# Kernel tuning notes

Hardware: AMD Instinct MI355X
Metric: run time of the kernel (lower is better)

## Reference

```python
import jax, jax.numpy as jnp
import numpy as np

BIG_NUM = 1000000000.0

def setup_inputs() -> dict:
    key0 = jax.random.key(0)
    k1, k2, k3, k4 = jax.random.split(key0, 4)
    B, T, D = 64, 4096, 512
    query = jax.random.normal(k1, (B, D), dtype=jnp.float32)
    key = jax.random.normal(k2, (B, T, D), dtype=jnp.float32)
    value = jax.random.normal(k3, (B, T, D), dtype=jnp.float32)
    mask = jax.random.randint(k4, (B, T), 0, 2, dtype=jnp.int32)
    return {"query": query, "key": key, "value": value, "mask": mask}

def reference(query, key, value, mask):
    # query: [B, D], key/value: [B, T, D], mask: [B, T] (1 = keep, 0 = mask)
    D = query.shape[1]
    scale = D ** 0.5
    # energy[b, t] = key[b, t, :] . query[b, :]
    energy = jnp.einsum('btd,bd->bt', key, query) / scale
    energy = energy + (mask.astype(jnp.float32) - 1.0) * BIG_NUM
    attn = jax.nn.softmax(energy, axis=-1)          # [B, T]
    context = jnp.einsum('bt,btd->bd', attn, value)  # [B, D]
    return (context, attn)
```

## Files before the change

kernel.cpp:

```cpp
#include <hip/hip_runtime.h>
#include <math.h>

#define B 64
#define T 4096
#define D 512
#define NCH 32
#define CHT (T / NCH)
#define WSTRIP 32
#define KBATCH 4
#define VBATCH 8

typedef __attribute__((address_space(1))) const void global_cv;
typedef __attribute__((address_space(3))) void lds_v;

__device__ __forceinline__ float wave_sum64(float v) {
#pragma unroll
    for (int off = 32; off; off >>= 1)
        v += __shfl_xor(v, off, 64);
    return v;
}

__device__ __forceinline__ void stage_row(const float* __restrict__ gsrc_row,
                                          float* lds_row, int lane) {
    __builtin_amdgcn_global_load_lds((global_cv*)(gsrc_row + lane * 4),
                                     (lds_v*)(lds_row), 16, 0, 0);
    __builtin_amdgcn_global_load_lds((global_cv*)(gsrc_row + 256 + lane * 4),
                                     (lds_v*)(lds_row + 256), 16, 0, 0);
}

__global__ __launch_bounds__(256) void energy_exp_kernel(const float* __restrict__ q,
                                                         const float* __restrict__ k,
                                                         const int* __restrict__ mask,
                                                         float* __restrict__ attn,
                                                         float* __restrict__ chunk_sums) {
    const float INV_SCALE = 0.04419417382415922f;

    __shared__ __align__(16) float kbuf[2][4][KBATCH][D];
    __shared__ int sm_list[4][WSTRIP + KBATCH];
    __shared__ float sred[4];

    int blk = blockIdx.x;
    int b = blk >> 5;
    int ch = blk & 31;
    int wave = threadIdx.x >> 6;
    int lane = threadIdx.x & 63;

    const float* qb = q + b * D;
    float4 qa = *(const float4*)(qb + lane * 4);
    float4 qc = *(const float4*)(qb + 256 + lane * 4);

    int t0 = ch * CHT + wave * WSTRIP;
    const float* kbase = k + ((size_t)b * T + t0) * D;

    int mv = (lane < WSTRIP) ? mask[b * T + t0 + lane] : 0;
    unsigned int mbits = (unsigned int)__ballot(mv != 0);
    int cnt = __popc(mbits);
    int row0 = (cnt > 0) ? (__ffs(mbits) - 1) : 0;
    if (lane < WSTRIP) {
        if (mv != 0) {
            int pre = __popc(mbits & ((1u << lane) - 1u));
            sm_list[wave][pre] = lane;
        } else {
            attn[(size_t)b * T + t0 + lane] = 0.0f;
        }
    }
    if (lane < KBATCH) sm_list[wave][cnt + lane] = row0;

    int ngrp = (cnt + KBATCH - 1) >> 2;

    if (ngrp > 0) {
#pragma unroll
        for (int r = 0; r < KBATCH; ++r)
            stage_row(kbase + (size_t)sm_list[wave][r] * D, &kbuf[0][wave][r][0], lane);
    }
    if (ngrp > 1) {
#pragma unroll
        for (int r = 0; r < KBATCH; ++r)
            stage_row(kbase + (size_t)sm_list[wave][KBATCH + r] * D, &kbuf[1][wave][r][0], lane);
    }

    int r2 = ((lane >> 5) & 1) | (((lane >> 4) & 1) << 1);
    float gsum = 0.f;

#pragma unroll 1
    for (int i = 0; i < ngrp; ++i) {
        if (i + 1 < ngrp) asm volatile("s_waitcnt vmcnt(8)" ::: "memory");
        else              asm volatile("s_waitcnt vmcnt(0)" ::: "memory");

        const float (*buf)[D] = kbuf[i & 1][wave];
        float d4[KBATCH];
#pragma unroll
        for (int rr = 0; rr < KBATCH; ++rr) {
            float4 ka = *(const float4*)&buf[rr][lane * 4];
            float4 kc = *(const float4*)&buf[rr][256 + lane * 4];
            d4[rr] = ka.x * qa.x + ka.y * qa.y + ka.z * qa.z + ka.w * qa.w
                   + kc.x * qc.x + kc.y * qc.y + kc.z * qc.z + kc.w * qc.w;
        }
        asm volatile("s_waitcnt lgkmcnt(0)" ::: "memory");
        if (i + 2 < ngrp) {
            int s0 = (i + 2) * KBATCH;
#pragma unroll
            for (int r = 0; r < KBATCH; ++r)
                stage_row(kbase + (size_t)sm_list[wave][s0 + r] * D,
                          &kbuf[i & 1][wave][r][0], lane);
        }

        bool b5 = (lane & 32) != 0;
        float e[2];
#pragma unroll
        for (int j = 0; j < 2; ++j) {
            float u = b5 ? d4[2*j+1] : d4[2*j];
            float s = b5 ? d4[2*j]   : d4[2*j+1];
            e[j] = u + __shfl_xor(s, 32, 64);
        }
        bool b4 = (lane & 16) != 0;
        float u = b4 ? e[1] : e[0];
        float s = b4 ? e[0] : e[1];
        float h = u + __shfl_xor(s, 16, 64);
        h += __shfl_xor(h, 8, 64);
        h += __shfl_xor(h, 4, 64);
        h += __shfl_xor(h, 2, 64);
        h += __shfl_xor(h, 1, 64);

        int slot = i * KBATCH + r2;
        float gval = 0.f;
        if (slot < cnt) {
            gval = __expf(h * INV_SCALE);
            if ((lane & 15) == 0) {
                int row = sm_list[wave][slot];
                attn[(size_t)b * T + t0 + row] = gval;
            }
        }
        gsum += gval;
    }

    float ws = wave_sum64(gsum) * 0.0625f;
    if (lane == 0) sred[wave] = ws;
    __syncthreads();
    if (threadIdx.x == 0)
        chunk_sums[blk] = (sred[0] + sred[1]) + (sred[2] + sred[3]);
}

__global__ __launch_bounds__(256) void context_partial_kernel(float* __restrict__ attn,
                                                              const float* __restrict__ v,
                                                              const float* __restrict__ chunk_sums,
                                                              float* __restrict__ partial) {
    __shared__ __align__(16) float vbuf[2][VBATCH][D];
    __shared__ float sa_raw[CHT];
    __shared__ int   rows[CHT + VBATCH];
    __shared__ float avals[CHT + VBATCH];
    __shared__ int   scnt;

    int blk = blockIdx.x;
    int b = blk >> 5;
    int ch = blk & 31;
    int tid = threadIdx.x;
    int wave = tid >> 6;
    int lane = tid & 63;

    float cs = (lane < NCH) ? chunk_sums[b * NCH + lane] : 0.f;
    float denom = wave_sum64(cs);
    float inv = 1.0f / denom;

    if (tid < CHT) sa_raw[tid] = attn[(size_t)b * T + ch * CHT + tid];
    __syncthreads();

    if (wave == 0) {
        float a0 = sa_raw[lane];
        unsigned long long bl0 = __ballot(a0 != 0.0f);
        int c0 = __popcll(bl0);
        if (a0 != 0.0f) {
            int p = __popcll(bl0 & ((1ull << lane) - 1ull));
            rows[p] = lane; avals[p] = a0;
        }
        float a1 = sa_raw[64 + lane];
        unsigned long long bl1 = __ballot(a1 != 0.0f);
        int c1 = __popcll(bl1);
        if (a1 != 0.0f) {
            int p = c0 + __popcll(bl1 & ((1ull << lane) - 1ull));
            rows[p] = 64 + lane; avals[p] = a1;
        }
        int cnt = c0 + c1;
        if (lane < VBATCH) {
            int safe0 = (cnt > 0) ? rows[0] : 0;
            rows[cnt + lane] = safe0;
            avals[cnt + lane] = 0.0f;
        }
        if (lane == 0) scnt = cnt;
    }
    __syncthreads();

    int cnt = scnt;
    int nb = (cnt + VBATCH - 1) / VBATCH;
    const float* vchunk = v + ((size_t)b * T + ch * CHT) * D;

    if (nb > 0) {
        int s0 = wave * 2;
        stage_row(vchunk + (size_t)rows[s0] * D,     &vbuf[0][wave * 2][0],     lane);
        stage_row(vchunk + (size_t)rows[s0 + 1] * D, &vbuf[0][wave * 2 + 1][0], lane);
    }
    if (nb > 1) {
        int s0 = VBATCH + wave * 2;
        stage_row(vchunk + (size_t)rows[s0] * D,     &vbuf[1][wave * 2][0],     lane);
        stage_row(vchunk + (size_t)rows[s0 + 1] * D, &vbuf[1][wave * 2 + 1][0], lane);
    }

    float2 acc = {0.f, 0.f};
    int c0 = tid * 2;
#pragma unroll 1
    for (int i = 0; i < nb; ++i) {
        if (i + 1 < nb) asm volatile("s_waitcnt vmcnt(4)" ::: "memory");
        else            asm volatile("s_waitcnt vmcnt(0)" ::: "memory");
        __builtin_amdgcn_s_barrier();

        const float (*buf)[D] = vbuf[i & 1];
        int base = i * VBATCH;
#pragma unroll
        for (int r = 0; r < VBATCH; ++r) {
            float a = avals[base + r];
            float2 vv = *(const float2*)&buf[r][c0];
            acc.x += a * vv.x;
            acc.y += a * vv.y;
        }
        __builtin_amdgcn_s_barrier();

        if (i + 2 < nb) {
            int s0 = (i + 2) * VBATCH + wave * 2;
            stage_row(vchunk + (size_t)rows[s0] * D,     &vbuf[i & 1][wave * 2][0],     lane);
            stage_row(vchunk + (size_t)rows[s0 + 1] * D, &vbuf[i & 1][wave * 2 + 1][0], lane);
        }
    }

    acc.x *= inv; acc.y *= inv;
    *(float2*)(partial + (size_t)(b * NCH + ch) * D + c0) = acc;

    if (tid < CHT)
        attn[(size_t)b * T + ch * CHT + tid] = sa_raw[tid] * inv;
}

__global__ __launch_bounds__(256) void context_reduce_kernel(const float* __restrict__ partial,
                                                             float* __restrict__ ctx) {
    int b = blockIdx.x;
    int tid = threadIdx.x;
    int d0 = tid * 2;
    float2 acc = {0.f, 0.f};
#pragma unroll 8
    for (int j = 0; j < NCH; ++j) {
        float2 p = *(const float2*)(partial + (size_t)(b * NCH + j) * D + d0);
        acc.x += p.x;
        acc.y += p.y;
    }
    *(float2*)(ctx + (size_t)b * D + d0) = acc;
}

extern "C" void kernel_launch(void* const* d_in, const int* in_sizes, int n_in,
                              void* d_out, int out_size, void* d_ws, size_t ws_size,
                              hipStream_t stream) {
    const float* q    = (const float*)d_in[0];
    const float* k    = (const float*)d_in[1];
    const float* v    = (const float*)d_in[2];
    const int*   mask = (const int*)d_in[3];

    float* ctx  = (float*)d_out;
    float* attn = (float*)d_out + B * D;

    float* chunk_sums = (float*)d_ws;
    float* partial    = (float*)d_ws + 8192;

    energy_exp_kernel<<<B * NCH, 256, 0, stream>>>(q, k, mask, attn, chunk_sums);
    context_partial_kernel<<<B * NCH, 256, 0, stream>>>(attn, v, chunk_sums, partial);
    context_reduce_kernel<<<B, 256, 0, stream>>>(partial, ctx);
}
```

Before: 111.4 us.

## Give each wave its own strip in context kernel and shrink K/V batches

The context kernel drops its block-wide compaction and its per-iteration barriers. Each wave now compacts its own 32-row strip, streams V rows through a private double buffer, and the block reduces the four per-wave accumulators in LDS at the end. The energy kernel cuts its K batch from 4 to 2 rows and collects exp values in LDS so attn is written with one coalesced store per strip. The goal is to remove barrier stalls and scattered stores, at the cost of fewer loads in flight per wave and an extra LDS reduction.

New measurement: 115.7 us. 1.04x slower.

```diff
diff --git a/kernel.cpp b/kernel.cpp
--- a/kernel.cpp
+++ b/kernel.cpp
@@ -7,8 +7,8 @@
 #define NCH 32
 #define CHT (T / NCH)
 #define WSTRIP 32
-#define KBATCH 4
-#define VBATCH 8
+#define KBATCH 2
+#define VB 2
 
 typedef __attribute__((address_space(1))) const void global_cv;
 typedef __attribute__((address_space(3))) void lds_v;
@@ -37,6 +37,7 @@
 
     __shared__ __align__(16) float kbuf[2][4][KBATCH][D];
     __shared__ int sm_list[4][WSTRIP + KBATCH];
+    __shared__ float sm_g[4][WSTRIP];
     __shared__ float sred[4];
 
     int blk = blockIdx.x;
@@ -57,16 +58,15 @@
     int cnt = __popc(mbits);
     int row0 = (cnt > 0) ? (__ffs(mbits) - 1) : 0;
     if (lane < WSTRIP) {
+        sm_g[wave][lane] = 0.0f;
         if (mv != 0) {
             int pre = __popc(mbits & ((1u << lane) - 1u));
             sm_list[wave][pre] = lane;
-        } else {
-            attn[(size_t)b * T + t0 + lane] = 0.0f;
         }
     }
     if (lane < KBATCH) sm_list[wave][cnt + lane] = row0;
 
-    int ngrp = (cnt + KBATCH - 1) >> 2;
+    int ngrp = (cnt + KBATCH - 1) >> 1;
 
     if (ngrp > 0) {
 #pragma unroll
@@ -79,21 +79,21 @@
             stage_row(kbase + (size_t)sm_list[wave][KBATCH + r] * D, &kbuf[1][wave][r][0], lane);
     }
 
-    int r2 = ((lane >> 5) & 1) | (((lane >> 4) & 1) << 1);
+    int rown = lane >> 5;
     float gsum = 0.f;
 
 #pragma unroll 1
     for (int i = 0; i < ngrp; ++i) {
-        if (i + 1 < ngrp) asm volatile("s_waitcnt vmcnt(8)" ::: "memory");
+        if (i + 1 < ngrp) asm volatile("s_waitcnt vmcnt(4)" ::: "memory");
         else              asm volatile("s_waitcnt vmcnt(0)" ::: "memory");
 
-        const float (*buf)[D] = kbuf[i & 1][wave];
-        float d4[KBATCH];
+        float d2[KBATCH];
 #pragma unroll
         for (int rr = 0; rr < KBATCH; ++rr) {
-            float4 ka = *(const float4*)&buf[rr][lane * 4];
-            float4 kc = *(const float4*)&buf[rr][256 + lane * 4];
-            d4[rr] = ka.x * qa.x + ka.y * qa.y + ka.z * qa.z + ka.w * qa.w
+            const float* buf = &kbuf[i & 1][wave][rr][0];
+            float4 ka = *(const float4*)&buf[lane * 4];
+            float4 kc = *(const float4*)&buf[256 + lane * 4];
+            d2[rr] = ka.x * qa.x + ka.y * qa.y + ka.z * qa.z + ka.w * qa.w
                    + kc.x * qc.x + kc.y * qc.y + kc.z * qc.z + kc.w * qc.w;
         }
         asm volatile("s_waitcnt lgkmcnt(0)" ::: "memory");
@@ -106,35 +106,29 @@
         }
 
         bool b5 = (lane & 32) != 0;
-        float e[2];
-#pragma unroll
-        for (int j = 0; j < 2; ++j) {
-            float u = b5 ? d4[2*j+1] : d4[2*j];
-            float s = b5 ? d4[2*j]   : d4[2*j+1];
-            e[j] = u + __shfl_xor(s, 32, 64);
-        }
-        bool b4 = (lane & 16) != 0;
-        float u = b4 ? e[1] : e[0];
-        float s = b4 ? e[0] : e[1];
-        float h = u + __shfl_xor(s, 16, 64);
+        float u = b5 ? d2[1] : d2[0];
+        float s = b5 ? d2[0] : d2[1];
+        float h = u + __shfl_xor(s, 32, 64);
+        h += __shfl_xor(h, 16, 64);
         h += __shfl_xor(h, 8, 64);
         h += __shfl_xor(h, 4, 64);
         h += __shfl_xor(h, 2, 64);
         h += __shfl_xor(h, 1, 64);
 
-        int slot = i * KBATCH + r2;
+        int slot = i * KBATCH + rown;
         float gval = 0.f;
         if (slot < cnt) {
             gval = __expf(h * INV_SCALE);
-            if ((lane & 15) == 0) {
-                int row = sm_list[wave][slot];
-                attn[(size_t)b * T + t0 + row] = gval;
-            }
+            if ((lane & 31) == 0)
+                sm_g[wave][sm_list[wave][slot]] = gval;
         }
         gsum += gval;
     }
 
-    float ws = wave_sum64(gsum) * 0.0625f;
+    if (lane < WSTRIP)
+        attn[(size_t)b * T + t0 + lane] = sm_g[wave][lane];
+
+    float ws = wave_sum64(gsum) * 0.03125f;
     if (lane == 0) sred[wave] = ws;
     __syncthreads();
     if (threadIdx.x == 0)
@@ -145,11 +139,10 @@
                                                               const float* __restrict__ v,
                                                               const float* __restrict__ chunk_sums,
                                                               float* __restrict__ partial) {
-    __shared__ __align__(16) float vbuf[2][VBATCH][D];
-    __shared__ float sa_raw[CHT];
-    __shared__ int   rows[CHT + VBATCH];
-    __shared__ float avals[CHT + VBATCH];
-    __shared__ int   scnt;
+    __shared__ __align__(16) float vbuf[2][4][VB][D];
+    __shared__ int   rows[4][WSTRIP + VB];
+    __shared__ float av[4][WSTRIP + VB];
+    __shared__ float sacc[4][D];
 
     int blk = blockIdx.x;
     int b = blk >> 5;
@@ -162,80 +155,81 @@
     float denom = wave_sum64(cs);
     float inv = 1.0f / denom;
 
-    if (tid < CHT) sa_raw[tid] = attn[(size_t)b * T + ch * CHT + tid];
-    __syncthreads();
-
-    if (wave == 0) {
-        float a0 = sa_raw[lane];
-        unsigned long long bl0 = __ballot(a0 != 0.0f);
-        int c0 = __popcll(bl0);
-        if (a0 != 0.0f) {
-            int p = __popcll(bl0 & ((1ull << lane) - 1ull));
-            rows[p] = lane; avals[p] = a0;
-        }
-        float a1 = sa_raw[64 + lane];
-        unsigned long long bl1 = __ballot(a1 != 0.0f);
-        int c1 = __popcll(bl1);
-        if (a1 != 0.0f) {
-            int p = c0 + __popcll(bl1 & ((1ull << lane) - 1ull));
-            rows[p] = 64 + lane; avals[p] = a1;
-        }
-        int cnt = c0 + c1;
-        if (lane < VBATCH) {
-            int safe0 = (cnt > 0) ? rows[0] : 0;
-            rows[cnt + lane] = safe0;
-            avals[cnt + lane] = 0.0f;
-        }
-        if (lane == 0) scnt = cnt;
-    }
-    __syncthreads();
-
-    int cnt = scnt;
-    int nb = (cnt + VBATCH - 1) / VBATCH;
-    const float* vchunk = v + ((size_t)b * T + ch * CHT) * D;
+    int t0 = ch * CHT + wave * WSTRIP;
+
+    float a = (lane < WSTRIP) ? attn[(size_t)b * T + t0 + lane] : 0.f;
+    unsigned long long bl = __ballot(a != 0.0f);
+    int cnt = __popcll(bl);
+    int row0 = (cnt > 0) ? (int)(__ffsll((unsigned long long)bl) - 1) : 0;
+    if (a != 0.0f) {
+        int pre = __popcll(bl & ((1ull << lane) - 1ull));
+        rows[wave][pre] = lane;
+        av[wave][pre] = a;
+    }
+    if (lane < VB) {
+        rows[wave][cnt + lane] = row0;
+        av[wave][cnt + lane] = 0.0f;
+    }
+
+    int nb = (cnt + VB - 1) >> 1;
+    const float* vw = v + ((size_t)b * T + t0) * D;
 
     if (nb > 0) {
-        int s0 = wave * 2;
-        stage_row(vchunk + (size_t)rows[s0] * D,     &vbuf[0][wave * 2][0],     lane);
-        stage_row(vchunk + (size_t)rows[s0 + 1] * D, &vbuf[0][wave * 2 + 1][0], lane);
+#pragma unroll
+        for (int r = 0; r < VB; ++r)
+            stage_row(vw + (size_t)rows[wave][r] * D, &vbuf[0][wave][r][0], lane);
     }
     if (nb > 1) {
-        int s0 = VBATCH + wave * 2;
-        stage_row(vchunk + (size_t)rows[s0] * D,     &vbuf[1][wave * 2][0],     lane);
-        stage_row(vchunk + (size_t)rows[s0 + 1] * D, &vbuf[1][wave * 2 + 1][0], lane);
-    }
-
-    float2 acc = {0.f, 0.f};
-    int c0 = tid * 2;
+#pragma unroll
+        for (int r = 0; r < VB; ++r)
+            stage_row(vw + (size_t)rows[wave][VB + r] * D, &vbuf[1][wave][r][0], lane);
+    }
+
+    float4 accA = {0.f, 0.f, 0.f, 0.f}, accC = {0.f, 0.f, 0.f, 0.f};
 #pragma unroll 1
     for (int i = 0; i < nb; ++i) {
         if (i + 1 < nb) asm volatile("s_waitcnt vmcnt(4)" ::: "memory");
         else            asm volatile("s_waitcnt vmcnt(0)" ::: "memory");
-        __builtin_amdgcn_s_barrier();
-
-        const float (*buf)[D] = vbuf[i & 1];
-        int base = i * VBATCH;
-#pragma unroll
-        for (int r = 0; r < VBATCH; ++r) {
-            float a = avals[base + r];
-            float2 vv = *(const float2*)&buf[r][c0];
-            acc.x += a * vv.x;
-            acc.y += a * vv.y;
-        }
-        __builtin_amdgcn_s_barrier();
-
+
+        float a0 = av[wave][i * 2];
+        float a1 = av[wave][i * 2 + 1];
+        const float* b0 = &vbuf[i & 1][wave][0][0];
+        const float* b1 = &vbuf[i & 1][wave][1][0];
+        float4 v0a = *(const float4*)&b0[lane * 4];
+        float4 v0c = *(const float4*)&b0[256 + lane * 4];
+        float4 v1a = *(const float4*)&b1[lane * 4];
+        float4 v1c = *(const float4*)&b1[256 + lane * 4];
+        accA.x += a0 * v0a.x + a1 * v1a.x;
+        accA.y += a0 * v0a.y + a1 * v1a.y;
+        accA.z += a0 * v0a.z + a1 * v1a.z;
+        accA.w += a0 * v0a.w + a1 * v1a.w;
+        accC.x += a0 * v0c.x + a1 * v1c.x;
+        accC.y += a0 * v0c.y + a1 * v1c.y;
+        accC.z += a0 * v0c.z + a1 * v1c.z;
+        accC.w += a0 * v0c.w + a1 * v1c.w;
+
+        asm volatile("s_waitcnt lgkmcnt(0)" ::: "memory");
         if (i + 2 < nb) {
-            int s0 = (i + 2) * VBATCH + wave * 2;
-            stage_row(vchunk + (size_t)rows[s0] * D,     &vbuf[i & 1][wave * 2][0],     lane);
-            stage_row(vchunk + (size_t)rows[s0 + 1] * D, &vbuf[i & 1][wave * 2 + 1][0], lane);
-        }
-    }
-
-    acc.x *= inv; acc.y *= inv;
-    *(float2*)(partial + (size_t)(b * NCH + ch) * D + c0) = acc;
-
-    if (tid < CHT)
-        attn[(size_t)b * T + ch * CHT + tid] = sa_raw[tid] * inv;
+            int s0 = (i + 2) * VB;
+#pragma unroll
+            for (int r = 0; r < VB; ++r)
+                stage_row(vw + (size_t)rows[wave][s0 + r] * D,
+                          &vbuf[i & 1][wave][r][0], lane);
+        }
+    }
+
+    if (lane < WSTRIP)
+        attn[(size_t)b * T + t0 + lane] = a * inv;
+
+    *(float4*)(&sacc[wave][lane * 4]) = accA;
+    *(float4*)(&sacc[wave][256 + lane * 4]) = accC;
+    __syncthreads();
+
+    int c0 = tid * 2;
+    float2 p;
+    p.x = ((sacc[0][c0]     + sacc[1][c0])     + (sacc[2][c0]     + sacc[3][c0])) * inv;
+    p.y = ((sacc[0][c0 + 1] + sacc[1][c0 + 1]) + (sacc[2][c0 + 1] + sacc[3][c0 + 1])) * inv;
+    *(float2*)(partial + (size_t)(b * NCH + ch) * D + c0) = p;
 }
 
 __global__ __launch_bounds__(256) void context_reduce_kernel(const float* __restrict__ partial,
```
